# Kernel optimization log

Measured on AMD Instinct MI355X. Metric: run time of the kernel, lower is better.

## Reference

```python
import jax, jax.numpy as jnp
import numpy as np

DIM, HEADS, K = 128, 4, 7
HD = DIM // HEADS


def _nbr_idx(n, k):
    # NATTEN boundary-clamped neighborhood (dilation=1): window start clamped to [0, n-k]
    i = np.arange(n)
    start = np.clip(i - k // 2, 0, n - k)
    idx = start[:, None] + np.arange(k)[None, :]          # (n, k) absolute neighbor index
    rel = idx - i[:, None] + (k - 1)                      # (n, k) index into 2k-1 rpb axis
    return jnp.asarray(idx), jnp.asarray(rel)


def _ln(x, w, b, eps=1e-5):
    mu = jnp.mean(x, -1, keepdims=True)
    var = jnp.var(x, -1, keepdims=True)
    return (x - mu) * jax.lax.rsqrt(var + eps) * w + b


def setup_inputs() -> dict:
    key = jax.random.key(0)
    ks = jax.random.split(key, 16)
    B, H, W, C = 1, 128, 128, DIM
    f = jax.random.normal
    inp = {
        'x': f(ks[0], (B, H, W, C), jnp.float32),
        'y': f(ks[1], (B, H, W, C), jnp.float32),
        'qv_w': f(ks[2], (2 * C, C), jnp.float32) * 0.02,
        'qv_b': jnp.zeros((2 * C,), jnp.float32),
        'k_w': f(ks[3], (C, C), jnp.float32) * 0.02,
        'k_b': jnp.zeros((C,), jnp.float32),
        'rpb': f(ks[4], (HEADS, 2 * K - 1, 2 * K - 1), jnp.float32) * 0.02,
        'proj_w': f(ks[5], (C, C), jnp.float32) * 0.02,
        'proj_b': jnp.zeros((C,), jnp.float32),
        'n1_w': jnp.ones((C,), jnp.float32),
        'n1_b': jnp.zeros((C,), jnp.float32),
        'n2_w': jnp.ones((C,), jnp.float32),
        'n2_b': jnp.zeros((C,), jnp.float32),
        'fc1_w': f(ks[6], (4 * C, C), jnp.float32) * 0.02,
        'fc1_b': jnp.zeros((4 * C,), jnp.float32),
        'fc2_w': f(ks[7], (C, 4 * C), jnp.float32) * 0.02,
        'fc2_b': jnp.zeros((C,), jnp.float32),
    }
    return inp


def _block(x, y, qv_w, qv_b, k_w, k_b, rpb, proj_w, proj_b,
           n1_w, n1_b, n2_w, n2_b, fc1_w, fc1_b, fc2_w, fc2_b):
    B, H, W, C = x.shape
    scale = HD ** -0.5
    # ---- CrossNat2D attention on norm1(x) vs y ----
    xn = _ln(x, n1_w, n1_b)
    qv = xn @ qv_w.T + qv_b                               # (B,H,W,2C)
    q = qv[..., :C].reshape(B, H, W, HEADS, HD) * scale
    v = qv[..., C:].reshape(B, H, W, HEADS, HD)
    k = (y @ k_w.T + k_b).reshape(B, H, W, HEADS, HD)

    idx_h, rel_h = _nbr_idx(H, K)
    idx_w, rel_w = _nbr_idx(W, K)
    # gather neighborhoods: (B, H, K, W, K, HEADS, HD)
    k_nbr = k[:, idx_h][:, :, :, idx_w]
    v_nbr = v[:, idx_h][:, :, :, idx_w]

    # attention logits over KxK neighborhood
    attn = jnp.einsum('bijhd,biajchd->bijhac', q, k_nbr)  # (B,H,W,heads,K,K)
    bias = rpb[:, rel_h][..., rel_w]                      # (heads,H,K,W,K)
    attn = attn + jnp.transpose(bias, (1, 3, 0, 2, 4))    # broadcast over B
    attn = jax.nn.softmax(attn.reshape(B, H, W, HEADS, K * K), axis=-1)
    attn = attn.reshape(B, H, W, HEADS, K, K)

    out = jnp.einsum('bijhac,biajchd->bijhd', attn, v_nbr).reshape(B, H, W, C)
    out = out @ proj_w.T + proj_b

    x = x + out
    # ---- MLP ----
    h = _ln(x, n2_w, n2_b) @ fc1_w.T + fc1_b
    h = jax.nn.gelu(h, approximate=False) @ fc2_w.T + fc2_b
    return x + h


def reference(x, y, qv_w, qv_b, k_w, k_b, rpb, proj_w, proj_b,
              n1_w, n1_b, n2_w, n2_b, fc1_w, fc1_b, fc2_w, fc2_b):
    return _block(x, y, qv_w, qv_b, k_w, k_b, rpb, proj_w, proj_b,
                  n1_w, n1_b, n2_w, n2_b, fc1_w, fc1_b, fc2_w, fc2_b)
```

## Files before the change

kernel.cpp:

```cpp
#include <hip/hip_runtime.h>
#include <hip/hip_bf16.h>


#define N_PIX 16384
#define C 128
#define HEADS 4
#define HD 32
#define HW 128

typedef __hip_bfloat16 bf16;
typedef __attribute__((ext_vector_type(8))) short bf16x8;
typedef __attribute__((ext_vector_type(4))) float f32x4;

__device__ __forceinline__ float b2f(bf16 v) { return __bfloat162float(v); }
__device__ __forceinline__ short f2bs(float f) {
    bf16 h = __float2bfloat16(f);
    return (short)__bfloat16_as_ushort(h);
}
__device__ __forceinline__ float bs2f(short s) {
    __hip_bfloat16_raw r; r.x = (unsigned short)s;
    return __bfloat162float(__hip_bfloat16(r));
}

__global__ __launch_bounds__(256) void k_wconv(
    const float* __restrict__ qv_w, const float* __restrict__ k_w,
    const float* __restrict__ proj_w, const float* __restrict__ fc1_w,
    const float* __restrict__ fc2_w,
    short* __restrict__ wqv, short* __restrict__ wk, short* __restrict__ wproj,
    short* __restrict__ wfc1, short* __restrict__ wfc2) {
    const int i = blockIdx.x * 256 + threadIdx.x;
    if (i < 32768) wqv[i] = f2bs(qv_w[i]);
    if (i < 16384) { wk[i] = f2bs(k_w[i]); wproj[i] = f2bs(proj_w[i]); }
    if (i < 65536) { wfc1[i] = f2bs(fc1_w[i]); wfc2[i] = f2bs(fc2_w[i]); }
}

__global__ __launch_bounds__(256) void k_qkv(
    const float* __restrict__ x, const float* __restrict__ y,
    const short* __restrict__ wqv, const float* __restrict__ qv_b,
    const short* __restrict__ wk, const float* __restrict__ k_b,
    const float* __restrict__ n1_w, const float* __restrict__ n1_b,
    bf16* __restrict__ qb, bf16* __restrict__ vb, bf16* __restrict__ kb) {
    __shared__ float xr[32][132];
    __shared__ short xn[32][136];
    __shared__ short yb[32][136];
    __shared__ float redS[32][8], redQ[32][8];
    __shared__ float muA[32], riA[32];
    const int t = threadIdx.x;
    const int pix0 = blockIdx.x * 32;
    for (int e = t; e < 32 * 128; e += 256) {
        const int r = e >> 7, c = e & 127;
        xr[r][c] = x[(pix0 + r) * C + c];
        yb[r][c] = f2bs(y[(pix0 + r) * C + c]);
    }
    __syncthreads();
    {
        const int r = t >> 3, s = t & 7;
        float sm = 0.f, sq = 0.f;
        for (int i = 0; i < 16; i++) { float v = xr[r][s * 16 + i]; sm += v; sq += v * v; }
        redS[r][s] = sm; redQ[r][s] = sq;
    }
    __syncthreads();
    if (t < 32) {
        float sm = 0.f, sq = 0.f;
        for (int s = 0; s < 8; s++) { sm += redS[t][s]; sq += redQ[t][s]; }
        const float mu = sm * (1.f / 128.f);
        const float var = sq * (1.f / 128.f) - mu * mu;
        muA[t] = mu; riA[t] = rsqrtf(var + 1e-5f);
    }
    __syncthreads();
    for (int e = t; e < 32 * 128; e += 256) {
        const int r = e >> 7, c = e & 127;
        xn[r][c] = f2bs((xr[r][c] - muA[r]) * riA[r] * n1_w[c] + n1_b[c]);
    }
    __syncthreads();
    const int wave = t >> 6, lane = t & 63, quad = lane >> 4, l15 = lane & 15;
    const float scale = 0.1767766952966369f;
    for (int jt = wave; jt < 48; jt += 4) {
        const int mt = jt & 1, nt = jt >> 1;
        f32x4 acc = {0.f, 0.f, 0.f, 0.f};
        if (nt < 16) {
            const int n = nt * 16 + l15;
            for (int kt = 0; kt < 4; kt++) {
                bf16x8 a = *(const bf16x8*)&xn[mt * 16 + l15][kt * 32 + quad * 8];
                bf16x8 b = *(const bf16x8*)&wqv[n * C + kt * 32 + quad * 8];
                acc = __builtin_amdgcn_mfma_f32_16x16x32_bf16(a, b, acc, 0, 0, 0);
            }
            const float bias = qv_b[n];
            for (int r = 0; r < 4; r++) {
                const int m = mt * 16 + quad * 4 + r;
                const float v = acc[r] + bias;
                if (n < C) qb[(pix0 + m) * C + n] = __float2bfloat16(v * scale);
                else       vb[(pix0 + m) * C + (n - C)] = __float2bfloat16(v);
            }
        } else {
            const int n = (nt - 16) * 16 + l15;
            for (int kt = 0; kt < 4; kt++) {
                bf16x8 a = *(const bf16x8*)&yb[mt * 16 + l15][kt * 32 + quad * 8];
                bf16x8 b = *(const bf16x8*)&wk[n * C + kt * 32 + quad * 8];
                acc = __builtin_amdgcn_mfma_f32_16x16x32_bf16(a, b, acc, 0, 0, 0);
            }
            const float bias = k_b[n];
            for (int r = 0; r < 4; r++) {
                const int m = mt * 16 + quad * 4 + r;
                kb[(pix0 + m) * C + n] = __float2bfloat16(acc[r] + bias);
            }
        }
    }
}

__global__ __launch_bounds__(256) void k_attn(
    const bf16* qb, const bf16* __restrict__ kb,
    const bf16* __restrict__ vb, const float* __restrict__ rpb,
    bf16* ao) {
    __shared__ short KP[112 * 136];
    __shared__ short Vl[112 * 136];
    __shared__ short rpbL[676];
    const int t = threadIdx.x;
    const int h = t >> 6, lane = t & 63, quad = lane >> 4, l15 = lane & 15;
    const int i0 = (blockIdx.x >> 4) * 2;
    const int j0 = (blockIdx.x & 15) * 8;
    const int rs = min(max(i0 - 3, 0), 120);
    const int cs = min(max(j0 - 3, 0), 114);
    for (int u = t; u < 112 * 16 * 2; u += 256) {
        const int tv = (u >= 1792) ? 1 : 0;
        const int uu = tv ? u - 1792 : u;
        const int r = uu >> 4, seg = uu & 15;
        const int wr = r / 14, wc = r % 14;
        const size_t g = (size_t)((rs + wr) * HW + cs + wc) * C + seg * 8;
        const uint4 d = *(const uint4*)((tv ? vb : kb) + g);
        *(uint4*)&(tv ? Vl : KP)[r * 136 + seg * 8] = d;
    }
    for (int u = t; u < 676; u += 256) rpbL[u] = f2bs(rpb[u]);
    __syncthreads();
    const int mA = l15;
    const int pA = (i0 + (mA >> 3)) * HW + j0 + (mA & 7);
    const bf16x8 aQ = *(const bf16x8*)(qb + (size_t)pA * C + h * HD + quad * 8);
    f32x4 S[7];
    for (int nt = 0; nt < 7; nt++) {
        const bf16x8 bK = *(const bf16x8*)&KP[(nt * 16 + l15) * 136 + h * HD + quad * 8];
        f32x4 z = {0.f, 0.f, 0.f, 0.f};
        S[nt] = __builtin_amdgcn_mfma_f32_16x16x32_bf16(aQ, bK, z, 0, 0, 0);
    }
    float mx[4], sm[4];
    for (int r = 0; r < 4; r++) {
        const int m = quad * 4 + r;
        const int i = i0 + (m >> 3), j = j0 + (m & 7);
        const int shi = min(max(i - 3, 0), 121);
        const int swj = min(max(j - 3, 0), 121);
        float best = -1e30f;
        for (int nt = 0; nt < 7; nt++) {
            const int nb = nt * 16 + l15;
            const int wr = nb / 14, wc = nb % 14;
            const int ai = rs + wr, aj = cs + wc;
            const bool valid = (ai >= shi) & (ai <= shi + 6) & (aj >= swj) & (aj <= swj + 6);
            const int ri = min(max(ai - i + 6, 0), 12);
            const int rj = min(max(aj - j + 6, 0), 12);
            const float bias = bs2f(rpbL[h * 169 + ri * 13 + rj]);
            const float v = valid ? (S[nt][r] + bias) : -1e30f;
            S[nt][r] = v;
            best = fmaxf(best, v);
        }
        for (int msk = 1; msk < 16; msk <<= 1) best = fmaxf(best, __shfl_xor(best, msk, 64));
        mx[r] = best;
        float s = 0.f;
        for (int nt = 0; nt < 7; nt++) {
            const float e = __expf(S[nt][r] - best);
            S[nt][r] = e;
            s += e;
        }
        for (int msk = 1; msk < 16; msk <<= 1) s += __shfl_xor(s, msk, 64);
        sm[r] = 1.f / s;
    }
    __syncthreads();
    for (int r = 0; r < 4; r++) {
        short* prow = &KP[(h * 16 + quad * 4 + r) * 136];
        for (int nt = 0; nt < 7; nt++)
            prow[nt * 16 + l15] = f2bs(S[nt][r] * sm[r]);
        prow[112 + l15] = 0;
    }
    __syncthreads();
    f32x4 O0 = {0.f, 0.f, 0.f, 0.f}, O1 = {0.f, 0.f, 0.f, 0.f};
    for (int kt = 0; kt < 4; kt++) {
        const bf16x8 aP = *(const bf16x8*)&KP[(h * 16 + l15) * 136 + kt * 32 + quad * 8];
        for (int nt2 = 0; nt2 < 2; nt2++) {
            bf16x8 bV;
            const int ch = h * HD + nt2 * 16 + l15;
#pragma unroll
            for (int jj = 0; jj < 8; jj++) {
                const int nbr = kt * 32 + quad * 8 + jj;
                bV[jj] = (nbr < 112) ? Vl[nbr * 136 + ch] : (short)0;
            }
            if (nt2 == 0) O0 = __builtin_amdgcn_mfma_f32_16x16x32_bf16(aP, bV, O0, 0, 0, 0);
            else          O1 = __builtin_amdgcn_mfma_f32_16x16x32_bf16(aP, bV, O1, 0, 0, 0);
        }
    }
    for (int r = 0; r < 4; r++) {
        const int m = quad * 4 + r;
        const int p = (i0 + (m >> 3)) * HW + j0 + (m & 7);
        ao[(size_t)p * C + h * HD + l15] = __float2bfloat16(O0[r]);
        ao[(size_t)p * C + h * HD + 16 + l15] = __float2bfloat16(O1[r]);
    }
}

__global__ __launch_bounds__(256) void k_mlp2(
    const float* __restrict__ x, const bf16* __restrict__ ao,
    const short* __restrict__ wproj, const float* __restrict__ proj_b,
    const float* __restrict__ n2_w, const float* __restrict__ n2_b,
    const short* __restrict__ wfc1, const float* __restrict__ fc1_b,
    const short* __restrict__ wfc2, const float* __restrict__ fc2_b,
    float* __restrict__ out) {
    __shared__ float xr[32][132];
    __shared__ short aos[32][136];
    __shared__ short xn[32][136];
    __shared__ short hb[32][520];
    __shared__ float redS[32][8], redQ[32][8];
    __shared__ float muA[32], riA[32];
    const int t = threadIdx.x;
    const int pix0 = blockIdx.x * 32;
    for (int e = t; e < 32 * 128; e += 256) {
        const int r = e >> 7, c = e & 127;
        xr[r][c] = x[(pix0 + r) * C + c];
    }
    for (int u = t; u < 32 * 16; u += 256) {
        const int r = u >> 4, seg = u & 15;
        *(uint4*)&aos[r][seg * 8] = *(const uint4*)(ao + (size_t)(pix0 + r) * C + seg * 8);
    }
    __syncthreads();
    const int wave = t >> 6, lane = t & 63, quad = lane >> 4, l15 = lane & 15;
    for (int jt = wave; jt < 16; jt += 4) {
        const int mt = jt >> 3, nt = jt & 7;
        const int n = nt * 16 + l15;
        f32x4 acc = {0.f, 0.f, 0.f, 0.f};
        for (int kt = 0; kt < 4; kt++) {
            bf16x8 a = *(const bf16x8*)&aos[mt * 16 + l15][kt * 32 + quad * 8];
            bf16x8 b = *(const bf16x8*)&wproj[n * C + kt * 32 + quad * 8];
            acc = __builtin_amdgcn_mfma_f32_16x16x32_bf16(a, b, acc, 0, 0, 0);
        }
        const float bias = proj_b[n];
        for (int r = 0; r < 4; r++) {
            const int m = mt * 16 + quad * 4 + r;
            xr[m][n] += acc[r] + bias;
        }
    }
    __syncthreads();
    {
        const int r = t >> 3, s = t & 7;
        float sm = 0.f, sq = 0.f;
        for (int i = 0; i < 16; i++) { float v = xr[r][s * 16 + i]; sm += v; sq += v * v; }
        redS[r][s] = sm; redQ[r][s] = sq;
    }
    __syncthreads();
    if (t < 32) {
        float sm = 0.f, sq = 0.f;
        for (int s = 0; s < 8; s++) { sm += redS[t][s]; sq += redQ[t][s]; }
        const float mu = sm * (1.f / 128.f);
        const float var = sq * (1.f / 128.f) - mu * mu;
        muA[t] = mu; riA[t] = rsqrtf(var + 1e-5f);
    }
    __syncthreads();
    for (int e = t; e < 32 * 128; e += 256) {
        const int r = e >> 7, c = e & 127;
        xn[r][c] = f2bs((xr[r][c] - muA[r]) * riA[r] * n2_w[c] + n2_b[c]);
    }
    __syncthreads();
    for (int jt = wave; jt < 64; jt += 4) {
        const int mt = jt >> 5, nt = jt & 31;
        const int n = nt * 16 + l15;
        f32x4 acc = {0.f, 0.f, 0.f, 0.f};
        for (int kt = 0; kt < 4; kt++) {
            bf16x8 a = *(const bf16x8*)&xn[mt * 16 + l15][kt * 32 + quad * 8];
            bf16x8 b = *(const bf16x8*)&wfc1[n * C + kt * 32 + quad * 8];
            acc = __builtin_amdgcn_mfma_f32_16x16x32_bf16(a, b, acc, 0, 0, 0);
        }
        const float bias = fc1_b[n];
        for (int r = 0; r < 4; r++) {
            const int m = mt * 16 + quad * 4 + r;
            float v = acc[r] + bias;
            v = 0.5f * v * (1.f + erff(v * 0.70710678118654752f));
            hb[m][n] = f2bs(v);
        }
    }
    __syncthreads();
    for (int jt = wave; jt < 16; jt += 4) {
        const int mt = jt >> 3, nt = jt & 7;
        const int n = nt * 16 + l15;
        f32x4 acc = {0.f, 0.f, 0.f, 0.f};
        for (int kt = 0; kt < 16; kt++) {
            bf16x8 a = *(const bf16x8*)&hb[mt * 16 + l15][kt * 32 + quad * 8];
            bf16x8 b = *(const bf16x8*)&wfc2[n * 512 + kt * 32 + quad * 8];
            acc = __builtin_amdgcn_mfma_f32_16x16x32_bf16(a, b, acc, 0, 0, 0);
        }
        const float bias = fc2_b[n];
        for (int r = 0; r < 4; r++) {
            const int m = mt * 16 + quad * 4 + r;
            out[(pix0 + m) * C + n] = acc[r] + bias + xr[m][n];
        }
    }
}

extern "C" void kernel_launch(void* const* d_in, const int* in_sizes, int n_in,
                              void* d_out, int out_size, void* d_ws, size_t ws_size,
                              hipStream_t stream) {
    const float* x      = (const float*)d_in[0];
    const float* y      = (const float*)d_in[1];
    const float* qv_w   = (const float*)d_in[2];
    const float* qv_b   = (const float*)d_in[3];
    const float* k_w    = (const float*)d_in[4];
    const float* k_b    = (const float*)d_in[5];
    const float* rpb    = (const float*)d_in[6];
    const float* proj_w = (const float*)d_in[7];
    const float* proj_b = (const float*)d_in[8];
    const float* n1_w   = (const float*)d_in[9];
    const float* n1_b   = (const float*)d_in[10];
    const float* n2_w   = (const float*)d_in[11];
    const float* n2_b   = (const float*)d_in[12];
    const float* fc1_w  = (const float*)d_in[13];
    const float* fc1_b  = (const float*)d_in[14];
    const float* fc2_w  = (const float*)d_in[15];
    const float* fc2_b  = (const float*)d_in[16];
    float* out = (float*)d_out;

    bf16* qb  = (bf16*)d_ws;
    bf16* vb  = qb + (size_t)N_PIX * C;
    bf16* kb  = vb + (size_t)N_PIX * C;
    short* wqv  = (short*)(kb + (size_t)N_PIX * C);
    short* wk   = wqv + 32768;
    short* wproj= wk + 16384;
    short* wfc1 = wproj + 16384;
    short* wfc2 = wfc1 + 65536;
    bf16* ao = qb;

    k_wconv<<<256, 256, 0, stream>>>(qv_w, k_w, proj_w, fc1_w, fc2_w,
                                     wqv, wk, wproj, wfc1, wfc2);
    k_qkv<<<N_PIX / 32, 256, 0, stream>>>(x, y, wqv, qv_b, wk, k_b, n1_w, n1_b, qb, vb, kb);
    k_attn<<<1024, 256, 0, stream>>>(qb, kb, vb, rpb, ao);
    k_mlp2<<<N_PIX / 32, 256, 0, stream>>>(x, ao, wproj, proj_b, n2_w, n2_b,
                                           wfc1, fc1_b, wfc2, fc2_b, out);
}
```

Measured before the change: 179.2 us.

## Use square 4x4 attention tiles, 512-thread QKV/MLP blocks, bf16 residual in LDS

Attention tiles change from 2x8 to 4x4 queries, so the staged K/V halo drops from 112 to 100 rows. The rpb table is now read straight from global memory instead of being staged in LDS. The QKV and MLP kernels move to 512 threads with 8 waves splitting the MFMA tiles. The MLP kernel reads the attention output directly from global memory and keeps the residual x1 as bf16 in LDS instead of fp32. This lowers LDS use and raises parallelism, but the residual now loses precision to bf16 rounding, which may hurt accuracy.

```diff
diff --git a/kernel.cpp b/kernel.cpp
--- a/kernel.cpp
+++ b/kernel.cpp
@@ -34,7 +34,7 @@
     if (i < 65536) { wfc1[i] = f2bs(fc1_w[i]); wfc2[i] = f2bs(fc2_w[i]); }
 }
 
-__global__ __launch_bounds__(256) void k_qkv(
+__global__ __launch_bounds__(512, 6) void k_qkv(
     const float* __restrict__ x, const float* __restrict__ y,
     const short* __restrict__ wqv, const float* __restrict__ qv_b,
     const short* __restrict__ wk, const float* __restrict__ k_b,
@@ -47,13 +47,13 @@
     __shared__ float muA[32], riA[32];
     const int t = threadIdx.x;
     const int pix0 = blockIdx.x * 32;
-    for (int e = t; e < 32 * 128; e += 256) {
+    for (int e = t; e < 32 * 128; e += 512) {
         const int r = e >> 7, c = e & 127;
         xr[r][c] = x[(pix0 + r) * C + c];
         yb[r][c] = f2bs(y[(pix0 + r) * C + c]);
     }
     __syncthreads();
-    {
+    if (t < 256) {
         const int r = t >> 3, s = t & 7;
         float sm = 0.f, sq = 0.f;
         for (int i = 0; i < 16; i++) { float v = xr[r][s * 16 + i]; sm += v; sq += v * v; }
@@ -68,14 +68,14 @@
         muA[t] = mu; riA[t] = rsqrtf(var + 1e-5f);
     }
     __syncthreads();
-    for (int e = t; e < 32 * 128; e += 256) {
+    for (int e = t; e < 32 * 128; e += 512) {
         const int r = e >> 7, c = e & 127;
         xn[r][c] = f2bs((xr[r][c] - muA[r]) * riA[r] * n1_w[c] + n1_b[c]);
     }
     __syncthreads();
     const int wave = t >> 6, lane = t & 63, quad = lane >> 4, l15 = lane & 15;
     const float scale = 0.1767766952966369f;
-    for (int jt = wave; jt < 48; jt += 4) {
+    for (int jt = wave; jt < 48; jt += 8) {
         const int mt = jt & 1, nt = jt >> 1;
         f32x4 acc = {0.f, 0.f, 0.f, 0.f};
         if (nt < 16) {
@@ -112,56 +112,55 @@
     const bf16* qb, const bf16* __restrict__ kb,
     const bf16* __restrict__ vb, const float* __restrict__ rpb,
     bf16* ao) {
-    __shared__ short KP[112 * 136];
-    __shared__ short Vl[112 * 136];
-    __shared__ short rpbL[676];
+    __shared__ short KP[100 * 132];
+    __shared__ short Vl[100 * 132];
     const int t = threadIdx.x;
     const int h = t >> 6, lane = t & 63, quad = lane >> 4, l15 = lane & 15;
-    const int i0 = (blockIdx.x >> 4) * 2;
-    const int j0 = (blockIdx.x & 15) * 8;
-    const int rs = min(max(i0 - 3, 0), 120);
-    const int cs = min(max(j0 - 3, 0), 114);
-    for (int u = t; u < 112 * 16 * 2; u += 256) {
-        const int tv = (u >= 1792) ? 1 : 0;
-        const int uu = tv ? u - 1792 : u;
+    const int i0 = (blockIdx.x >> 5) * 4;
+    const int j0 = (blockIdx.x & 31) * 4;
+    const int rs = min(max(i0 - 3, 0), 118);
+    const int cs = min(max(j0 - 3, 0), 118);
+    for (int u = t; u < 100 * 16 * 2; u += 256) {
+        const int tv = (u >= 1600) ? 1 : 0;
+        const int uu = tv ? u - 1600 : u;
         const int r = uu >> 4, seg = uu & 15;
-        const int wr = r / 14, wc = r % 14;
+        const int wr = r / 10, wc = r % 10;
         const size_t g = (size_t)((rs + wr) * HW + cs + wc) * C + seg * 8;
         const uint4 d = *(const uint4*)((tv ? vb : kb) + g);
-        *(uint4*)&(tv ? Vl : KP)[r * 136 + seg * 8] = d;
-    }
-    for (int u = t; u < 676; u += 256) rpbL[u] = f2bs(rpb[u]);
-    __syncthreads();
-    const int mA = l15;
-    const int pA = (i0 + (mA >> 3)) * HW + j0 + (mA & 7);
+        *(uint4*)&(tv ? Vl : KP)[r * 132 + seg * 8] = d;
+    }
+    __syncthreads();
+    const int pA = (i0 + (l15 >> 2)) * HW + j0 + (l15 & 3);
     const bf16x8 aQ = *(const bf16x8*)(qb + (size_t)pA * C + h * HD + quad * 8);
     f32x4 S[7];
+    int aiL[7], ajL[7]; bool inb[7];
     for (int nt = 0; nt < 7; nt++) {
-        const bf16x8 bK = *(const bf16x8*)&KP[(nt * 16 + l15) * 136 + h * HD + quad * 8];
+        const int nb = nt * 16 + l15;
+        aiL[nt] = rs + nb / 10;
+        ajL[nt] = cs + nb % 10;
+        inb[nt] = nb < 100;
+        const bf16x8 bK = *(const bf16x8*)&KP[(nt * 16 + l15) * 132 + h * HD + quad * 8];
         f32x4 z = {0.f, 0.f, 0.f, 0.f};
         S[nt] = __builtin_amdgcn_mfma_f32_16x16x32_bf16(aQ, bK, z, 0, 0, 0);
     }
-    float mx[4], sm[4];
+    const float* rpbh = rpb + h * 169;
+    float sm[4];
     for (int r = 0; r < 4; r++) {
         const int m = quad * 4 + r;
-        const int i = i0 + (m >> 3), j = j0 + (m & 7);
+        const int i = i0 + (m >> 2), j = j0 + (m & 3);
         const int shi = min(max(i - 3, 0), 121);
         const int swj = min(max(j - 3, 0), 121);
         float best = -1e30f;
         for (int nt = 0; nt < 7; nt++) {
-            const int nb = nt * 16 + l15;
-            const int wr = nb / 14, wc = nb % 14;
-            const int ai = rs + wr, aj = cs + wc;
-            const bool valid = (ai >= shi) & (ai <= shi + 6) & (aj >= swj) & (aj <= swj + 6);
+            const int ai = aiL[nt], aj = ajL[nt];
+            const bool valid = inb[nt] & (ai >= shi) & (ai <= shi + 6) & (aj >= swj) & (aj <= swj + 6);
             const int ri = min(max(ai - i + 6, 0), 12);
             const int rj = min(max(aj - j + 6, 0), 12);
-            const float bias = bs2f(rpbL[h * 169 + ri * 13 + rj]);
-            const float v = valid ? (S[nt][r] + bias) : -1e30f;
+            const float v = valid ? (S[nt][r] + rpbh[ri * 13 + rj]) : -1e30f;
             S[nt][r] = v;
             best = fmaxf(best, v);
         }
         for (int msk = 1; msk < 16; msk <<= 1) best = fmaxf(best, __shfl_xor(best, msk, 64));
-        mx[r] = best;
         float s = 0.f;
         for (int nt = 0; nt < 7; nt++) {
             const float e = __expf(S[nt][r] - best);
@@ -188,7 +187,7 @@
 #pragma unroll
             for (int jj = 0; jj < 8; jj++) {
                 const int nbr = kt * 32 + quad * 8 + jj;
-                bV[jj] = (nbr < 112) ? Vl[nbr * 136 + ch] : (short)0;
+                bV[jj] = (nbr < 100) ? Vl[nbr * 132 + ch] : (short)0;
             }
             if (nt2 == 0) O0 = __builtin_amdgcn_mfma_f32_16x16x32_bf16(aP, bV, O0, 0, 0, 0);
             else          O1 = __builtin_amdgcn_mfma_f32_16x16x32_bf16(aP, bV, O1, 0, 0, 0);
@@ -196,57 +195,48 @@
     }
     for (int r = 0; r < 4; r++) {
         const int m = quad * 4 + r;
-        const int p = (i0 + (m >> 3)) * HW + j0 + (m & 7);
+        const int p = (i0 + (m >> 2)) * HW + j0 + (m & 3);
         ao[(size_t)p * C + h * HD + l15] = __float2bfloat16(O0[r]);
         ao[(size_t)p * C + h * HD + 16 + l15] = __float2bfloat16(O1[r]);
     }
 }
 
-__global__ __launch_bounds__(256) void k_mlp2(
+__global__ __launch_bounds__(512, 6) void k_mlp2(
     const float* __restrict__ x, const bf16* __restrict__ ao,
     const short* __restrict__ wproj, const float* __restrict__ proj_b,
     const float* __restrict__ n2_w, const float* __restrict__ n2_b,
     const short* __restrict__ wfc1, const float* __restrict__ fc1_b,
     const short* __restrict__ wfc2, const float* __restrict__ fc2_b,
     float* __restrict__ out) {
-    __shared__ float xr[32][132];
-    __shared__ short aos[32][136];
+    __shared__ short x1b[32][136];
     __shared__ short xn[32][136];
     __shared__ short hb[32][520];
     __shared__ float redS[32][8], redQ[32][8];
     __shared__ float muA[32], riA[32];
     const int t = threadIdx.x;
     const int pix0 = blockIdx.x * 32;
-    for (int e = t; e < 32 * 128; e += 256) {
-        const int r = e >> 7, c = e & 127;
-        xr[r][c] = x[(pix0 + r) * C + c];
-    }
-    for (int u = t; u < 32 * 16; u += 256) {
-        const int r = u >> 4, seg = u & 15;
-        *(uint4*)&aos[r][seg * 8] = *(const uint4*)(ao + (size_t)(pix0 + r) * C + seg * 8);
-    }
-    __syncthreads();
     const int wave = t >> 6, lane = t & 63, quad = lane >> 4, l15 = lane & 15;
-    for (int jt = wave; jt < 16; jt += 4) {
+    for (int jt = wave; jt < 16; jt += 8) {
         const int mt = jt >> 3, nt = jt & 7;
         const int n = nt * 16 + l15;
+        const bf16* aop = ao + (size_t)(pix0 + mt * 16 + l15) * C;
         f32x4 acc = {0.f, 0.f, 0.f, 0.f};
         for (int kt = 0; kt < 4; kt++) {
-            bf16x8 a = *(const bf16x8*)&aos[mt * 16 + l15][kt * 32 + quad * 8];
+            bf16x8 a = *(const bf16x8*)(aop + kt * 32 + quad * 8);
             bf16x8 b = *(const bf16x8*)&wproj[n * C + kt * 32 + quad * 8];
             acc = __builtin_amdgcn_mfma_f32_16x16x32_bf16(a, b, acc, 0, 0, 0);
         }
         const float bias = proj_b[n];
         for (int r = 0; r < 4; r++) {
             const int m = mt * 16 + quad * 4 + r;
-            xr[m][n] += acc[r] + bias;
-        }
-    }
-    __syncthreads();
-    {
+            x1b[m][n] = f2bs(x[(pix0 + m) * C + n] + acc[r] + bias);
+        }
+    }
+    __syncthreads();
+    if (t < 256) {
         const int r = t >> 3, s = t & 7;
         float sm = 0.f, sq = 0.f;
-        for (int i = 0; i < 16; i++) { float v = xr[r][s * 16 + i]; sm += v; sq += v * v; }
+        for (int i = 0; i < 16; i++) { float v = bs2f(x1b[r][s * 16 + i]); sm += v; sq += v * v; }
         redS[r][s] = sm; redQ[r][s] = sq;
     }
     __syncthreads();
@@ -258,12 +248,12 @@
         muA[t] = mu; riA[t] = rsqrtf(var + 1e-5f);
     }
     __syncthreads();
-    for (int e = t; e < 32 * 128; e += 256) {
+    for (int e = t; e < 32 * 128; e += 512) {
         const int r = e >> 7, c = e & 127;
-        xn[r][c] = f2bs((xr[r][c] - muA[r]) * riA[r] * n2_w[c] + n2_b[c]);
-    }
-    __syncthreads();
-    for (int jt = wave; jt < 64; jt += 4) {
+        xn[r][c] = f2bs((bs2f(x1b[r][c]) - muA[r]) * riA[r] * n2_w[c] + n2_b[c]);
+    }
+    __syncthreads();
+    for (int jt = wave; jt < 64; jt += 8) {
         const int mt = jt >> 5, nt = jt & 31;
         const int n = nt * 16 + l15;
         f32x4 acc = {0.f, 0.f, 0.f, 0.f};
@@ -281,7 +271,7 @@
         }
     }
     __syncthreads();
-    for (int jt = wave; jt < 16; jt += 4) {
+    for (int jt = wave; jt < 16; jt += 8) {
         const int mt = jt >> 3, nt = jt & 7;
         const int n = nt * 16 + l15;
         f32x4 acc = {0.f, 0.f, 0.f, 0.f};
@@ -293,7 +283,7 @@
         const float bias = fc2_b[n];
         for (int r = 0; r < 4; r++) {
             const int m = mt * 16 + quad * 4 + r;
-            out[(pix0 + m) * C + n] = acc[r] + bias + xr[m][n];
+            out[(pix0 + m) * C + n] = acc[r] + bias + bs2f(x1b[m][n]);
         }
     }
 }
@@ -332,8 +322,8 @@
 
     k_wconv<<<256, 256, 0, stream>>>(qv_w, k_w, proj_w, fc1_w, fc2_w,
                                      wqv, wk, wproj, wfc1, wfc2);
-    k_qkv<<<N_PIX / 32, 256, 0, stream>>>(x, y, wqv, qv_b, wk, k_b, n1_w, n1_b, qb, vb, kb);
+    k_qkv<<<N_PIX / 32, 512, 0, stream>>>(x, y, wqv, qv_b, wk, k_b, n1_w, n1_b, qb, vb, kb);
     k_attn<<<1024, 256, 0, stream>>>(qb, kb, vb, rpb, ao);
-    k_mlp2<<<N_PIX / 32, 256, 0, stream>>>(x, ao, wproj, proj_b, n2_w, n2_b,
+    k_mlp2<<<N_PIX / 32, 512, 0, stream>>>(x, ao, wproj, proj_b, n2_w, n2_b,
                                            wfc1, fc1_b, wfc2, fc2_b, out);
 }
```

Result: no change. 176.2 us (-1.7%).
